# Performance work log

Hardware: AMD Instinct MI355X
Metric: run time of the kernel (lower is better)

The kernel has to match this reference:

```python
import jax, jax.numpy as jnp
import numpy as np

DATA_WIDTH = 416.0
IOU_THRESH = 0.5
TOPK = 1024  # fixed-size candidate set to keep shapes static (replaces dynamic nonzero/filter)


def setup_inputs() -> dict:
    key = jax.random.key(0)
    ks = jax.random.split(key, 6)
    B, C = 32, 255  # 3 anchors * (5 + 80 classes)
    return {
        "out_13": jax.random.normal(ks[0], (B, C, 13, 13), jnp.float32),
        "out_26": jax.random.normal(ks[1], (B, C, 26, 26), jnp.float32),
        "out_52": jax.random.normal(ks[2], (B, C, 52, 52), jnp.float32),
        "thresh_value": jnp.float32(0.0),
        "case": jnp.float32(1.0),
        "anchors_13": jax.random.uniform(ks[3], (3, 2), jnp.float32) * 100.0 + 10.0,
        "anchors_26": jax.random.uniform(ks[4], (3, 2), jnp.float32) * 50.0 + 5.0,
        "anchors_52": jax.random.uniform(ks[5], (3, 2), jnp.float32) * 25.0 + 2.0,
    }


def _decode(out, thresh, anchors, t, case):
    # out: [B, 3*(5+nc), G, G] -> [B, G, G, 3, 5+nc]  (matches permute+reshape in _filter)
    B, ch, G, _ = out.shape
    out = jnp.transpose(out, (0, 2, 3, 1)).reshape(B, G, G, 3, -1)
    conf = jax.nn.sigmoid(out[..., 0])                         # sigmoid(p)
    iy = jnp.arange(G, dtype=out.dtype)[None, :, None, None]   # idxs[:,1]
    ix = jnp.arange(G, dtype=out.dtype)[None, None, :, None]   # idxs[:,2]
    # NOTE: original code uses vecs[:, 2] for BOTH cy and cx (replicated faithfully)
    cy = (iy + out[..., 2]) * t / case
    cx = (ix + out[..., 2]) * t / case
    w = anchors[:, 0] * jnp.exp(out[..., 3]) / case            # broadcast over anchor dim
    h = anchors[:, 1] * jnp.exp(out[..., 4]) / case
    cls_p = jax.nn.softmax(out[..., 5:], axis=-1)
    cls = jnp.argmax(cls_p, axis=-1).astype(out.dtype)
    n = jnp.broadcast_to(jnp.arange(B, dtype=out.dtype)[:, None, None, None], conf.shape)
    boxes = jnp.stack([n, conf, cx, cy, w, h, cls], axis=-1).reshape(-1, 7)
    # threshold filter (mask = sigmoid(p) > thresh), expressed as masked score for static shapes
    score = jnp.where(conf > thresh, conf, -1.0).reshape(-1)
    return boxes, score


def _nms_keep(boxes, score):
    # boxes: [K, 7] rows [n, p, cx, cy, w, h, cls]; greedy NMS, IoU = inter/union ('inter' mode)
    K = boxes.shape[0]
    cx, cy, w, h = boxes[:, 2], boxes[:, 3], boxes[:, 4], boxes[:, 5]
    x1, y1, x2, y2 = cx - w / 2, cy - h / 2, cx + w / 2, cy + h / 2
    area = w * h
    iw = jnp.clip(jnp.minimum(x2[:, None], x2[None, :]) - jnp.maximum(x1[:, None], x1[None, :]), 0.0)
    ih = jnp.clip(jnp.minimum(y2[:, None], y2[None, :]) - jnp.maximum(y1[:, None], y1[None, :]), 0.0)
    inter = iw * ih
    iou = inter / (area[:, None] + area[None, :] - inter + 1e-9)
    idx = jnp.arange(K)
    supp0 = score <= 0.0  # padding / below-threshold entries start suppressed

    def body(i, supp):
        row = (~supp[i]) & (iou[i] > IOU_THRESH) & (idx > i)
        return supp | row

    supp = jax.lax.fori_loop(0, K, body, supp0)
    return ~supp


def reference(out_13, out_26, out_52, thresh_value, case, anchors_13, anchors_26, anchors_52):
    b13, s13 = _decode(out_13, thresh_value, anchors_13, DATA_WIDTH / 13, case)
    b26, s26 = _decode(out_26, thresh_value, anchors_26, DATA_WIDTH / 26, case)
    b52, s52 = _decode(out_52, thresh_value, anchors_52, DATA_WIDTH / 52, case)
    boxes = jnp.concatenate([b13, b26, b52], axis=0)
    score = jnp.concatenate([s13, s26, s52], axis=0)
    topv, topi = jax.lax.top_k(score, TOPK)          # confidence-sorted candidates
    boxes_k = boxes[topi]
    keep = jax.lax.stop_gradient(_nms_keep(boxes_k, topv))
    return boxes_k * keep[:, None].astype(boxes_k.dtype)  # [TOPK, 7], suppressed rows zeroed
```

## Files before the change

kernel.cpp:

```cpp
#include <hip/hip_runtime.h>
#include <math.h>

typedef unsigned int u32;
typedef unsigned long long u64;

#define N_13 16224
#define N_26 64896
#define N_52 259584
#define N_TOT 340704
#define KSEL 1024
#define NBINS 8192
#define NBH 64
#define CAND 2048

#define WS_HIST 0UL
#define WS_STK  32768UL
#define WS_CAND 32784UL
#define WS_GATH 49168UL
#define WS_BOX7 57360UL
#define WS_X1   86032UL
#define WS_Y1   90128UL
#define WS_X2   94224UL
#define WS_Y2   98320UL
#define WS_AR   102416UL
#define WS_SUP  106512UL
#define WS_MASK 110608UL

__device__ __forceinline__ float sigmoid_(float x) {
  return 1.0f / (1.0f + expf(-x));
}

__device__ __forceinline__ u32 fkey_(float f) {
  u32 u = __float_as_uint(f);
  return (u & 0x80000000u) ? ~u : (u | 0x80000000u);
}

__device__ __forceinline__ int binof_(float l0, float score) {
  if (score == -1.0f) return 0;
  int b = (int)floorf((l0 + 8.0f) * 512.0f);
  return b < 0 ? 0 : (b > NBINS-1 ? NBINS-1 : b);
}

__device__ __forceinline__ const float* level_(int t, const float* f13,
                                               const float* f26, const float* f52,
                                               int& G2, int& off, int& tl) {
  if (t < N_13)            { G2 = 169;  off = 0;         tl = t;                return f13; }
  else if (t < N_13+N_26)  { G2 = 676;  off = N_13;      tl = t - N_13;         return f26; }
  else                     { G2 = 2704; off = N_13+N_26; tl = t - (N_13+N_26);  return f52; }
}

__global__ __launch_bounds__(1024) void hist_kernel(const float* __restrict__ f13,
                                                    const float* __restrict__ f26,
                                                    const float* __restrict__ f52,
                                                    const float* __restrict__ thr_p,
                                                    u32* __restrict__ hist) {
  __shared__ u32 lh[NBINS];
  int tid = threadIdx.x;
  for (int i = tid; i < NBINS; i += 1024) lh[i] = 0u;
  __syncthreads();
  float thr = *thr_p;
  for (int t = blockIdx.x * 1024 + tid; t < N_TOT; t += NBH * 1024) {
    int G2, off, tl;
    const float* fp = level_(t, f13, f26, f52, G2, off, tl);
    int p = tl % G2; int c = tl / G2; int a = c % 3; int b = c / 3;
    float l0 = fp[(size_t)(b*255 + a*85) * G2 + p];
    float conf = sigmoid_(l0);
    float score = (conf > thr) ? conf : -1.0f;
    atomicAdd(&lh[binof_(l0, score)], 1u);
  }
  __syncthreads();
  for (int i = tid; i < NBINS; i += 1024) {
    u32 v = lh[i];
    if (v) atomicAdd(&hist[i], v);
  }
}

__global__ __launch_bounds__(1024) void pick_kernel(const u32* __restrict__ hist,
                                                    u32* __restrict__ stk,
                                                    u64* __restrict__ cand) {
  __shared__ u32 lh[NBINS];
  __shared__ u32 suf[1024];
  int t = threadIdx.x;
  u32 s = 0;
  #pragma unroll 8
  for (int d = 0; d < 8; ++d) { u32 v = hist[t*8 + d]; lh[t*8 + d] = v; s += v; }
  suf[t] = s;
  __syncthreads();
  for (int off = 1; off < 1024; off <<= 1) {
    u32 v = (t + off < 1024) ? suf[t + off] : 0u;
    __syncthreads();
    suf[t] += v;
    __syncthreads();
  }
  if (suf[t] >= (u32)KSEL && (t == 1023 || suf[t+1] < (u32)KSEL)) {
    u32 cum = (t < 1023) ? suf[t+1] : 0u;
    int bsel = t*8;
    for (int d = 7; d >= 0; --d) {
      cum += lh[t*8 + d];
      if (cum >= (u32)KSEL) { bsel = t*8 + d; break; }
    }
    stk[1] = (u32)bsel;
  }
  cand[t] = 0ull; cand[t + 1024] = 0ull;
}

__global__ void gather_kernel(const float* __restrict__ f13,
                              const float* __restrict__ f26,
                              const float* __restrict__ f52,
                              const float* __restrict__ thr_p,
                              u32* __restrict__ stk, u64* __restrict__ cand) {
  int t = blockIdx.x * blockDim.x + threadIdx.x;
  if (t >= N_TOT) return;
  float thr = *thr_p;
  int G2, off, tl;
  const float* fp = level_(t, f13, f26, f52, G2, off, tl);
  int p = tl % G2; int c = tl / G2; int a = c % 3; int b = c / 3;
  float l0 = fp[(size_t)(b*255 + a*85) * G2 + p];
  float conf = sigmoid_(l0);
  float score = (conf > thr) ? conf : -1.0f;
  int bin = binof_(l0, score);
  if ((u32)bin >= stk[1]) {
    u32 iref = (u32)(off + (b*G2 + p)*3 + a);
    u64 key = ((u64)fkey_(score) << 19) | (u64)(524287u - iref);
    u32 pos = atomicAdd(&stk[0], 1u);
    if (pos < (u32)CAND) cand[pos] = key;
  }
}

__global__ __launch_bounds__(1024) void sort_kernel(const u64* __restrict__ cand,
                                                    u64* __restrict__ gath) {
  __shared__ u64 sk[CAND];
  int t = threadIdx.x;
  sk[t] = cand[t]; sk[t + 1024] = cand[t + 1024];
  __syncthreads();
  for (int kk = 2; kk <= CAND; kk <<= 1) {
    for (int j = kk >> 1; j > 0; j >>= 1) {
      #pragma unroll
      for (int h = 0; h < 2; ++h) {
        int e = t + h*1024;
        int ixj = e ^ j;
        if (ixj > e) {
          u64 x0 = sk[e], x1 = sk[ixj];
          bool descRegion = (e & kk) == 0;
          bool sw = descRegion ? (x0 < x1) : (x0 > x1);
          if (sw) { sk[e] = x1; sk[ixj] = x0; }
        }
      }
      __syncthreads();
    }
  }
  gath[t] = sk[t];
}

__global__ void decode_kernel(const float* __restrict__ f13,
                              const float* __restrict__ f26,
                              const float* __restrict__ f52,
                              const float* __restrict__ a13,
                              const float* __restrict__ a26,
                              const float* __restrict__ a52,
                              const float* __restrict__ case_p,
                              const u64* __restrict__ gath,
                              float* __restrict__ box7,
                              float* __restrict__ bx1, float* __restrict__ by1,
                              float* __restrict__ bx2, float* __restrict__ by2,
                              float* __restrict__ bar, u32* __restrict__ bsup) {
  int gt = blockIdx.x * blockDim.x + threadIdx.x;
  int r = gt >> 6;
  int lane = gt & 63;
  if (r >= KSEL) return;
  u64 key = gath[r];
  u32 idx = 524287u - ((u32)key & 0x7FFFFu);
  u32 sb = (u32)(key >> 19);
  sb = (sb & 0x80000000u) ? (sb & 0x7FFFFFFFu) : ~sb;
  float score = __uint_as_float(sb);
  float case_v = *case_p;

  const float* fp; const float* ap; u32 G, G2, off; float tt;
  if (idx < N_13)            { fp=f13; ap=a13; G=13; G2=169;  off=0;          tt=32.0f; }
  else if (idx < N_13+N_26)  { fp=f26; ap=a26; G=26; G2=676;  off=N_13;       tt=16.0f; }
  else                       { fp=f52; ap=a52; G=52; G2=2704; off=N_13+N_26;  tt=8.0f;  }
  u32 L = idx - off;
  u32 a = L % 3u; u32 q = L / 3u;
  u32 x = q % G; u32 rq = q / G; u32 y = rq % G; u32 b = rq / G;

  const float* base = fp + (size_t)(b*255u + a*85u) * G2 + y*G + x;
  float l0 = base[0];
  float conf = sigmoid_(l0);
  float l2 = base[(size_t)2*G2];
  float l3 = base[(size_t)3*G2];
  float l4 = base[(size_t)4*G2];
  float cy = ((float)y + l2) * tt / case_v;
  float cx = ((float)x + l2) * tt / case_v;
  float w = ap[2*a]     * expf(l3) / case_v;
  float h = ap[2*a + 1] * expf(l4) / case_v;

  bool v2ok = (lane < 16);
  float x1 = base[(size_t)(5 + lane) * G2];
  float x2 = v2ok ? base[(size_t)(5 + 64 + lane) * G2] : -INFINITY;
  float mx = fmaxf(x1, x2);
  #pragma unroll
  for (int o = 32; o > 0; o >>= 1) mx = fmaxf(mx, __shfl_xor(mx, o));
  float e1 = expf(x1 - mx);
  float e2 = v2ok ? expf(x2 - mx) : 0.0f;
  float ssum = e1 + e2;
  #pragma unroll
  for (int o = 32; o > 0; o >>= 1) ssum += __shfl_xor(ssum, o);
  float p1 = e1 / ssum;
  float p2 = v2ok ? (e2 / ssum) : -1.0f;
  float pm = p1; int ci = lane;
  if (p2 > pm) { pm = p2; ci = lane + 64; }
  #pragma unroll
  for (int o = 32; o > 0; o >>= 1) {
    float om = __shfl_xor(pm, o);
    int   oc = __shfl_xor(ci, o);
    if (om > pm || (om == pm && oc < ci)) { pm = om; ci = oc; }
  }

  if (lane == 0) {
    box7[r*7 + 0] = (float)b;
    box7[r*7 + 1] = conf;
    box7[r*7 + 2] = cx;
    box7[r*7 + 3] = cy;
    box7[r*7 + 4] = w;
    box7[r*7 + 5] = h;
    box7[r*7 + 6] = (float)ci;
    float hw = __fmul_rn(w, 0.5f);
    float hh = __fmul_rn(h, 0.5f);
    bx1[r] = __fsub_rn(cx, hw);
    bx2[r] = __fadd_rn(cx, hw);
    by1[r] = __fsub_rn(cy, hh);
    by2[r] = __fadd_rn(cy, hh);
    bar[r] = __fmul_rn(w, h);
    bsup[r] = (score <= 0.0f) ? 1u : 0u;
  }
}

__global__ __launch_bounds__(256) void mask_kernel(const float* __restrict__ bx1,
                                                   const float* __restrict__ by1,
                                                   const float* __restrict__ bx2,
                                                   const float* __restrict__ by2,
                                                   const float* __restrict__ bar,
                                                   u64* __restrict__ mask) {
  __shared__ float sx1[1024], sy1[1024], sx2[1024], sy2[1024], sar[1024];
  int t = threadIdx.x;
  for (int k = t; k < 1024; k += 256) {
    sx1[k] = bx1[k]; sy1[k] = by1[k];
    sx2[k] = bx2[k]; sy2[k] = by2[k]; sar[k] = bar[k];
  }
  __syncthreads();
  int T = blockIdx.x * 256 + t;
  int i = T >> 4, w = T & 15;
  float x1 = sx1[i], y1 = sy1[i], x2 = sx2[i], y2 = sy2[i], ar = sar[i];
  u64 m = 0;
  int j0 = w << 6;
  for (int b = 0; b < 64; ++b) {
    int j = j0 + b;
    float iw = fmaxf(__fsub_rn(fminf(sx2[j], x2), fmaxf(sx1[j], x1)), 0.0f);
    float ih = fmaxf(__fsub_rn(fminf(sy2[j], y2), fmaxf(sy1[j], y1)), 0.0f);
    float inter = __fmul_rn(iw, ih);
    float den = __fadd_rn(__fsub_rn(__fadd_rn(ar, sar[j]), inter), 1e-9f);
    float iou = inter / den;
    if (iou > 0.5f && j > i) m |= (1ull << b);
  }
  mask[i*16 + w] = m;
}

__global__ __launch_bounds__(1024) void resolve_kernel(const u64* __restrict__ mask,
                                                       const u32* __restrict__ bsup,
                                                       const float* __restrict__ box7,
                                                       float* __restrict__ out) {
  __shared__ u64 sm[16384];
  __shared__ u64 ssupw[16];
  int t = threadIdx.x;
  for (int k = t; k < 16384; k += 1024) sm[k] = mask[k];
  __syncthreads();
  if (t < 64) {
    int lane = t;
    u64 supp = 0;
    for (int w = 0; w < 16; ++w) {
      u64 bal = __ballot(bsup[w*64 + lane] != 0u);
      if (w == lane) supp = bal;
    }
    u64 c0, c1, c2, c3, n0, n1, n2, n3;
    c0 = (lane < 16) ? sm[0*16 + lane] : 0ull;
    c1 = (lane < 16) ? sm[1*16 + lane] : 0ull;
    c2 = (lane < 16) ? sm[2*16 + lane] : 0ull;
    c3 = (lane < 16) ? sm[3*16 + lane] : 0ull;
    for (int i = 0; i < 1024; i += 4) {
      if (i + 4 < 1024) {
        n0 = (lane < 16) ? sm[(i+4)*16 + lane] : 0ull;
        n1 = (lane < 16) ? sm[(i+5)*16 + lane] : 0ull;
        n2 = (lane < 16) ? sm[(i+6)*16 + lane] : 0ull;
        n3 = (lane < 16) ? sm[(i+7)*16 + lane] : 0ull;
      } else { n0 = n1 = n2 = n3 = 0ull; }
      u64 sw;
      sw = __shfl(supp, (i  ) >> 6); if (!((sw >> ((i  ) & 63)) & 1ull)) supp |= c0;
      sw = __shfl(supp, (i+1) >> 6); if (!((sw >> ((i+1) & 63)) & 1ull)) supp |= c1;
      sw = __shfl(supp, (i+2) >> 6); if (!((sw >> ((i+2) & 63)) & 1ull)) supp |= c2;
      sw = __shfl(supp, (i+3) >> 6); if (!((sw >> ((i+3) & 63)) & 1ull)) supp |= c3;
      c0 = n0; c1 = n1; c2 = n2; c3 = n3;
    }
    if (lane < 16) ssupw[lane] = supp;
  }
  __syncthreads();
  u32 keep = !((ssupw[t >> 6] >> (t & 63)) & 1ull);
  #pragma unroll
  for (int c = 0; c < 7; ++c) {
    float v = box7[t*7 + c];
    out[t*7 + c] = keep ? v : 0.0f;
  }
}

extern "C" void kernel_launch(void* const* d_in, const int* in_sizes, int n_in,
                              void* d_out, int out_size, void* d_ws, size_t ws_size,
                              hipStream_t stream) {
  const float* f13 = (const float*)d_in[0];
  const float* f26 = (const float*)d_in[1];
  const float* f52 = (const float*)d_in[2];
  const float* thr = (const float*)d_in[3];
  const float* cas = (const float*)d_in[4];
  const float* a13 = (const float*)d_in[5];
  const float* a26 = (const float*)d_in[6];
  const float* a52 = (const float*)d_in[7];
  float* out = (float*)d_out;
  char* ws = (char*)d_ws;

  u32* hist = (u32*)(ws + WS_HIST);
  u32* stk  = (u32*)(ws + WS_STK);
  u64* cand = (u64*)(ws + WS_CAND);
  u64* gath = (u64*)(ws + WS_GATH);
  float* box7 = (float*)(ws + WS_BOX7);
  float* bx1 = (float*)(ws + WS_X1);
  float* by1 = (float*)(ws + WS_Y1);
  float* bx2 = (float*)(ws + WS_X2);
  float* by2 = (float*)(ws + WS_Y2);
  float* bar = (float*)(ws + WS_AR);
  u32* bsup = (u32*)(ws + WS_SUP);
  u64* mask = (u64*)(ws + WS_MASK);

  const int nb = (N_TOT + 255) / 256;

  hipMemsetAsync(ws + WS_HIST, 0, 32768 + 16, stream);
  hist_kernel<<<NBH, 1024, 0, stream>>>(f13, f26, f52, thr, hist);
  pick_kernel<<<1, 1024, 0, stream>>>(hist, stk, cand);
  gather_kernel<<<nb, 256, 0, stream>>>(f13, f26, f52, thr, stk, cand);
  sort_kernel<<<1, 1024, 0, stream>>>(cand, gath);
  decode_kernel<<<256, 256, 0, stream>>>(f13, f26, f52, a13, a26, a52, cas, gath,
                                         box7, bx1, by1, bx2, by2, bar, bsup);
  mask_kernel<<<64, 256, 0, stream>>>(bx1, by1, bx2, by2, bar, mask);
  resolve_kernel<<<1, 1024, 0, stream>>>(mask, bsup, box7, out);
}
```

Measured before the change: 281.4 us.

## Fuse NMS pipeline into single cooperative kernel with grid syncs

Replaces seven kernel launches and a memset with one cooperative kernel of 64 blocks that separates the stages with grid.sync. The bitonic sort becomes a parallel rank-by-count sort spread across blocks. The resolve step now works on 32-bit words using readlane, and the histogram loops are specialised per level through templates. The aim is to remove launch and inter-kernel gaps; the cost is grid-wide barriers and having the whole pipeline use only 64 blocks.

```diff
diff --git a/kernel.cpp b/kernel.cpp
--- a/kernel.cpp
+++ b/kernel.cpp
@@ -1,5 +1,8 @@
 #include <hip/hip_runtime.h>
+#include <hip/hip_cooperative_groups.h>
 #include <math.h>
+
+namespace cg = cooperative_groups;
 
 typedef unsigned int u32;
 typedef unsigned long long u64;
@@ -10,8 +13,10 @@
 #define N_TOT 340704
 #define KSEL 1024
 #define NBINS 8192
-#define NBH 64
 #define CAND 2048
+#define NBLK 64
+#define NTHR 1024
+#define GSTRIDE (NBLK * NTHR)
 
 #define WS_HIST 0UL
 #define WS_STK  32768UL
@@ -41,273 +46,271 @@
   return b < 0 ? 0 : (b > NBINS-1 ? NBINS-1 : b);
 }
 
-__device__ __forceinline__ const float* level_(int t, const float* f13,
-                                               const float* f26, const float* f52,
-                                               int& G2, int& off, int& tl) {
-  if (t < N_13)            { G2 = 169;  off = 0;         tl = t;                return f13; }
-  else if (t < N_13+N_26)  { G2 = 676;  off = N_13;      tl = t - N_13;         return f26; }
-  else                     { G2 = 2704; off = N_13+N_26; tl = t - (N_13+N_26);  return f52; }
-}
-
-__global__ __launch_bounds__(1024) void hist_kernel(const float* __restrict__ f13,
-                                                    const float* __restrict__ f26,
-                                                    const float* __restrict__ f52,
-                                                    const float* __restrict__ thr_p,
-                                                    u32* __restrict__ hist) {
-  __shared__ u32 lh[NBINS];
-  int tid = threadIdx.x;
-  for (int i = tid; i < NBINS; i += 1024) lh[i] = 0u;
-  __syncthreads();
-  float thr = *thr_p;
-  for (int t = blockIdx.x * 1024 + tid; t < N_TOT; t += NBH * 1024) {
-    int G2, off, tl;
-    const float* fp = level_(t, f13, f26, f52, G2, off, tl);
-    int p = tl % G2; int c = tl / G2; int a = c % 3; int b = c / 3;
-    float l0 = fp[(size_t)(b*255 + a*85) * G2 + p];
-    float conf = sigmoid_(l0);
-    float score = (conf > thr) ? conf : -1.0f;
-    atomicAdd(&lh[binof_(l0, score)], 1u);
-  }
-  __syncthreads();
-  for (int i = tid; i < NBINS; i += 1024) {
-    u32 v = lh[i];
-    if (v) atomicAdd(&hist[i], v);
-  }
-}
-
-__global__ __launch_bounds__(1024) void pick_kernel(const u32* __restrict__ hist,
-                                                    u32* __restrict__ stk,
-                                                    u64* __restrict__ cand) {
-  __shared__ u32 lh[NBINS];
-  __shared__ u32 suf[1024];
-  int t = threadIdx.x;
-  u32 s = 0;
-  #pragma unroll 8
-  for (int d = 0; d < 8; ++d) { u32 v = hist[t*8 + d]; lh[t*8 + d] = v; s += v; }
-  suf[t] = s;
-  __syncthreads();
-  for (int off = 1; off < 1024; off <<= 1) {
-    u32 v = (t + off < 1024) ? suf[t + off] : 0u;
-    __syncthreads();
-    suf[t] += v;
-    __syncthreads();
-  }
-  if (suf[t] >= (u32)KSEL && (t == 1023 || suf[t+1] < (u32)KSEL)) {
-    u32 cum = (t < 1023) ? suf[t+1] : 0u;
-    int bsel = t*8;
-    for (int d = 7; d >= 0; --d) {
-      cum += lh[t*8 + d];
-      if (cum >= (u32)KSEL) { bsel = t*8 + d; break; }
-    }
-    stk[1] = (u32)bsel;
-  }
-  cand[t] = 0ull; cand[t + 1024] = 0ull;
-}
-
-__global__ void gather_kernel(const float* __restrict__ f13,
-                              const float* __restrict__ f26,
-                              const float* __restrict__ f52,
-                              const float* __restrict__ thr_p,
-                              u32* __restrict__ stk, u64* __restrict__ cand) {
-  int t = blockIdx.x * blockDim.x + threadIdx.x;
-  if (t >= N_TOT) return;
-  float thr = *thr_p;
-  int G2, off, tl;
-  const float* fp = level_(t, f13, f26, f52, G2, off, tl);
-  int p = tl % G2; int c = tl / G2; int a = c % 3; int b = c / 3;
+template<int G2>
+__device__ __forceinline__ void hist_item(const float* __restrict__ fp, int u,
+                                          float thr, u32* lh) {
+  int p = u % G2; int c = u / G2; int a = c % 3; int b = c / 3;
+  float l0 = fp[(size_t)(b*255 + a*85) * G2 + p];
+  float conf = sigmoid_(l0);
+  float score = (conf > thr) ? conf : -1.0f;
+  atomicAdd(&lh[binof_(l0, score)], 1u);
+}
+
+template<int G2, int OFF>
+__device__ __forceinline__ void gather_item(const float* __restrict__ fp, int u,
+                                            float thr, u32 bsel,
+                                            u32* stk, u64* cand) {
+  int p = u % G2; int c = u / G2; int a = c % 3; int b = c / 3;
   float l0 = fp[(size_t)(b*255 + a*85) * G2 + p];
   float conf = sigmoid_(l0);
   float score = (conf > thr) ? conf : -1.0f;
   int bin = binof_(l0, score);
-  if ((u32)bin >= stk[1]) {
-    u32 iref = (u32)(off + (b*G2 + p)*3 + a);
+  if ((u32)bin >= bsel) {
+    u32 iref = (u32)(OFF + (b*G2 + p)*3 + a);
     u64 key = ((u64)fkey_(score) << 19) | (u64)(524287u - iref);
     u32 pos = atomicAdd(&stk[0], 1u);
     if (pos < (u32)CAND) cand[pos] = key;
   }
 }
 
-__global__ __launch_bounds__(1024) void sort_kernel(const u64* __restrict__ cand,
-                                                    u64* __restrict__ gath) {
-  __shared__ u64 sk[CAND];
-  int t = threadIdx.x;
-  sk[t] = cand[t]; sk[t + 1024] = cand[t + 1024];
+union SmemT {
+  u32 lh[NBINS];
+  u32 wsum[16];
+  u64 sk[CAND];
+  struct { float x1[1024], y1[1024], x2[1024], y2[1024], ar[1024]; } mk;
+  struct { u32 sm32[33280]; u32 sw[32]; } rs;
+};
+
+__global__ __launch_bounds__(NTHR) void fused_kernel(
+    const float* __restrict__ f13, const float* __restrict__ f26,
+    const float* __restrict__ f52, const float* __restrict__ thr_p,
+    const float* __restrict__ case_p, const float* __restrict__ a13,
+    const float* __restrict__ a26, const float* __restrict__ a52,
+    float* __restrict__ out, char* __restrict__ ws) {
+  __shared__ SmemT sm;
+  cg::grid_group grid = cg::this_grid();
+
+  u32* hist = (u32*)(ws + WS_HIST);
+  u32* stk  = (u32*)(ws + WS_STK);
+  u64* cand = (u64*)(ws + WS_CAND);
+  u64* gath = (u64*)(ws + WS_GATH);
+  float* box7 = (float*)(ws + WS_BOX7);
+  float* bx1 = (float*)(ws + WS_X1);
+  float* by1 = (float*)(ws + WS_Y1);
+  float* bx2 = (float*)(ws + WS_X2);
+  float* by2 = (float*)(ws + WS_Y2);
+  float* bar = (float*)(ws + WS_AR);
+  u32* bsup = (u32*)(ws + WS_SUP);
+  u64* mask = (u64*)(ws + WS_MASK);
+
+  const int tid = threadIdx.x;
+  const int gtid = blockIdx.x * NTHR + tid;
+
+  for (int i = tid; i < NBINS; i += NTHR) sm.lh[i] = 0u;
   __syncthreads();
-  for (int kk = 2; kk <= CAND; kk <<= 1) {
-    for (int j = kk >> 1; j > 0; j >>= 1) {
+  if (gtid < NBINS) hist[gtid] = 0u;
+  if (gtid < 4) stk[gtid] = 0u;
+  if (gtid < CAND) cand[gtid] = 0ull;
+  {
+    float thr = *thr_p;
+    for (int u = gtid; u < N_13; u += GSTRIDE) hist_item<169 >(f13, u, thr, sm.lh);
+    for (int u = gtid; u < N_26; u += GSTRIDE) hist_item<676 >(f26, u, thr, sm.lh);
+    for (int u = gtid; u < N_52; u += GSTRIDE) hist_item<2704>(f52, u, thr, sm.lh);
+  }
+  __syncthreads();
+  grid.sync();
+
+  for (int i = tid; i < NBINS; i += NTHR) {
+    u32 v = sm.lh[i];
+    if (v) atomicAdd(&hist[i], v);
+  }
+  grid.sync();
+
+  if (blockIdx.x == 0) {
+    u32 h[8]; u32 s = 0;
+    #pragma unroll
+    for (int d = 0; d < 8; ++d) { h[d] = hist[tid*8 + d]; s += h[d]; }
+    u32 r = s;
+    #pragma unroll
+    for (int off = 1; off < 64; off <<= 1) {
+      u32 v = __shfl_down(r, off);
+      if ((tid & 63) + off < 64) r += v;
+    }
+    if ((tid & 63) == 0) sm.wsum[tid >> 6] = r;
+    __syncthreads();
+    u32 add = 0;
+    for (int w2 = (tid >> 6) + 1; w2 < 16; ++w2) add += sm.wsum[w2];
+    u32 suf = r + add;
+    if (suf >= (u32)KSEL && (suf - s) < (u32)KSEL) {
+      u32 cum = suf - s;
+      int bsel = tid*8;
+      for (int d = 7; d >= 0; --d) {
+        cum += h[d];
+        if (cum >= (u32)KSEL) { bsel = tid*8 + d; break; }
+      }
+      stk[1] = (u32)bsel;
+    }
+  }
+  grid.sync();
+
+  {
+    float thr = *thr_p;
+    u32 bsel = stk[1];
+    for (int u = gtid; u < N_13; u += GSTRIDE) gather_item<169 , 0          >(f13, u, thr, bsel, stk, cand);
+    for (int u = gtid; u < N_26; u += GSTRIDE) gather_item<676 , N_13      >(f26, u, thr, bsel, stk, cand);
+    for (int u = gtid; u < N_52; u += GSTRIDE) gather_item<2704, N_13+N_26 >(f52, u, thr, bsel, stk, cand);
+  }
+  grid.sync();
+
+  {
+    for (int k = tid; k < CAND; k += NTHR) sm.sk[k] = cand[k];
+    __syncthreads();
+    int e = blockIdx.x * 32 + (tid >> 5);
+    int sub = tid & 31;
+    u64 mykey = sm.sk[e];
+    u32 cnt = 0;
+    for (int s = 0; s < 64; ++s) {
+      int j = sub*64 + ((s + sub) & 63);
+      cnt += (sm.sk[j] > mykey) ? 1u : 0u;
+    }
+    #pragma unroll
+    for (int off = 1; off < 32; off <<= 1) cnt += __shfl_xor(cnt, off);
+    if (sub == 0 && cnt < (u32)KSEL) gath[cnt] = mykey;
+  }
+  grid.sync();
+
+  {
+    int r = blockIdx.x * 16 + (tid >> 6);
+    int lane = tid & 63;
+    u64 key = gath[r];
+    u32 idx = 524287u - ((u32)key & 0x7FFFFu);
+    u32 sb = (u32)(key >> 19);
+    sb = (sb & 0x80000000u) ? (sb & 0x7FFFFFFFu) : ~sb;
+    float score = __uint_as_float(sb);
+    float case_v = *case_p;
+
+    const float* fp; const float* ap; u32 G, G2, off; float tt;
+    if (idx < N_13)            { fp=f13; ap=a13; G=13; G2=169;  off=0;          tt=32.0f; }
+    else if (idx < N_13+N_26)  { fp=f26; ap=a26; G=26; G2=676;  off=N_13;       tt=16.0f; }
+    else                       { fp=f52; ap=a52; G=52; G2=2704; off=N_13+N_26;  tt=8.0f;  }
+    u32 L = idx - off;
+    u32 a = L % 3u; u32 q = L / 3u;
+    u32 x = q % G; u32 rq = q / G; u32 y = rq % G; u32 b = rq / G;
+
+    const float* base = fp + (size_t)(b*255u + a*85u) * G2 + y*G + x;
+    float l0 = base[0];
+    float conf = sigmoid_(l0);
+    float l2 = base[(size_t)2*G2];
+    float l3 = base[(size_t)3*G2];
+    float l4 = base[(size_t)4*G2];
+    float cy = ((float)y + l2) * tt / case_v;
+    float cx = ((float)x + l2) * tt / case_v;
+    float w = ap[2*a]     * expf(l3) / case_v;
+    float h = ap[2*a + 1] * expf(l4) / case_v;
+
+    bool v2ok = (lane < 16);
+    float x1v = base[(size_t)(5 + lane) * G2];
+    float x2v = v2ok ? base[(size_t)(5 + 64 + lane) * G2] : -INFINITY;
+    float mx = fmaxf(x1v, x2v);
+    #pragma unroll
+    for (int o = 32; o > 0; o >>= 1) mx = fmaxf(mx, __shfl_xor(mx, o));
+    float e1 = expf(x1v - mx);
+    float e2 = v2ok ? expf(x2v - mx) : 0.0f;
+    float ssum = e1 + e2;
+    #pragma unroll
+    for (int o = 32; o > 0; o >>= 1) ssum += __shfl_xor(ssum, o);
+    float p1 = e1 / ssum;
+    float p2 = v2ok ? (e2 / ssum) : -1.0f;
+    float pm = p1; int ci = lane;
+    if (p2 > pm) { pm = p2; ci = lane + 64; }
+    #pragma unroll
+    for (int o = 32; o > 0; o >>= 1) {
+      float om = __shfl_xor(pm, o);
+      int   oc = __shfl_xor(ci, o);
+      if (om > pm || (om == pm && oc < ci)) { pm = om; ci = oc; }
+    }
+
+    if (lane == 0) {
+      box7[r*7 + 0] = (float)b;
+      box7[r*7 + 1] = conf;
+      box7[r*7 + 2] = cx;
+      box7[r*7 + 3] = cy;
+      box7[r*7 + 4] = w;
+      box7[r*7 + 5] = h;
+      box7[r*7 + 6] = (float)ci;
+      float hw = __fmul_rn(w, 0.5f);
+      float hh = __fmul_rn(h, 0.5f);
+      bx1[r] = __fsub_rn(cx, hw);
+      bx2[r] = __fadd_rn(cx, hw);
+      by1[r] = __fsub_rn(cy, hh);
+      by2[r] = __fadd_rn(cy, hh);
+      bar[r] = __fmul_rn(w, h);
+      bsup[r] = (score <= 0.0f) ? 1u : 0u;
+    }
+  }
+  grid.sync();
+
+  if (blockIdx.x < 16) {
+    sm.mk.x1[tid] = bx1[tid]; sm.mk.y1[tid] = by1[tid];
+    sm.mk.x2[tid] = bx2[tid]; sm.mk.y2[tid] = by2[tid];
+    sm.mk.ar[tid] = bar[tid];
+    __syncthreads();
+    int P = blockIdx.x * NTHR + tid;
+    int i = P >> 4, w = P & 15;
+    float x1 = sm.mk.x1[i], y1 = sm.mk.y1[i];
+    float x2 = sm.mk.x2[i], y2 = sm.mk.y2[i], ar = sm.mk.ar[i];
+    u64 m = 0;
+    int j0 = w << 6;
+    for (int b = 0; b < 64; ++b) {
+      int j = j0 + b;
+      float iw = fmaxf(__fsub_rn(fminf(sm.mk.x2[j], x2), fmaxf(sm.mk.x1[j], x1)), 0.0f);
+      float ih = fmaxf(__fsub_rn(fminf(sm.mk.y2[j], y2), fmaxf(sm.mk.y1[j], y1)), 0.0f);
+      float inter = __fmul_rn(iw, ih);
+      float den = __fadd_rn(__fsub_rn(__fadd_rn(ar, sm.mk.ar[j]), inter), 1e-9f);
+      float iou = inter / den;
+      if (iou > 0.5f && j > i) m |= (1ull << b);
+    }
+    mask[i*16 + w] = m;
+  }
+  grid.sync();
+
+  if (blockIdx.x == 0) {
+    u64* smask = (u64*)sm.rs.sm32;
+    for (int k = tid; k < 16384; k += NTHR) smask[k] = mask[k];
+    if (tid < 256) smask[16384 + tid] = 0ull;
+    if (tid < 32) sm.rs.sw[tid] = 0u;
+    __syncthreads();
+    if (bsup[tid]) atomicOr(&sm.rs.sw[tid >> 5], 1u << (tid & 31));
+    __syncthreads();
+    if (tid < 64) {
+      int lane = tid;
+      bool act = lane < 32;
+      u32 supp = act ? sm.rs.sw[lane] : 0u;
+      u32 cur[8], nxt[8];
       #pragma unroll
-      for (int h = 0; h < 2; ++h) {
-        int e = t + h*1024;
-        int ixj = e ^ j;
-        if (ixj > e) {
-          u64 x0 = sk[e], x1 = sk[ixj];
-          bool descRegion = (e & kk) == 0;
-          bool sw = descRegion ? (x0 < x1) : (x0 > x1);
-          if (sw) { sk[e] = x1; sk[ixj] = x0; }
+      for (int k = 0; k < 8; ++k) cur[k] = act ? sm.rs.sm32[k*32 + lane] : 0u;
+      for (int blk = 0; blk < 128; ++blk) {
+        #pragma unroll
+        for (int k = 0; k < 8; ++k)
+          nxt[k] = act ? sm.rs.sm32[(blk*8 + 8 + k)*32 + lane] : 0u;
+        #pragma unroll
+        for (int k = 0; k < 8; ++k) {
+          int i = blk*8 + k;
+          u32 swd = (u32)__builtin_amdgcn_readlane((int)supp, i >> 5);
+          if (!((swd >> (i & 31)) & 1u)) supp |= cur[k];
         }
+        #pragma unroll
+        for (int k = 0; k < 8; ++k) cur[k] = nxt[k];
       }
-      __syncthreads();
-    }
-  }
-  gath[t] = sk[t];
-}
-
-__global__ void decode_kernel(const float* __restrict__ f13,
-                              const float* __restrict__ f26,
-                              const float* __restrict__ f52,
-                              const float* __restrict__ a13,
-                              const float* __restrict__ a26,
-                              const float* __restrict__ a52,
-                              const float* __restrict__ case_p,
-                              const u64* __restrict__ gath,
-                              float* __restrict__ box7,
-                              float* __restrict__ bx1, float* __restrict__ by1,
-                              float* __restrict__ bx2, float* __restrict__ by2,
-                              float* __restrict__ bar, u32* __restrict__ bsup) {
-  int gt = blockIdx.x * blockDim.x + threadIdx.x;
-  int r = gt >> 6;
-  int lane = gt & 63;
-  if (r >= KSEL) return;
-  u64 key = gath[r];
-  u32 idx = 524287u - ((u32)key & 0x7FFFFu);
-  u32 sb = (u32)(key >> 19);
-  sb = (sb & 0x80000000u) ? (sb & 0x7FFFFFFFu) : ~sb;
-  float score = __uint_as_float(sb);
-  float case_v = *case_p;
-
-  const float* fp; const float* ap; u32 G, G2, off; float tt;
-  if (idx < N_13)            { fp=f13; ap=a13; G=13; G2=169;  off=0;          tt=32.0f; }
-  else if (idx < N_13+N_26)  { fp=f26; ap=a26; G=26; G2=676;  off=N_13;       tt=16.0f; }
-  else                       { fp=f52; ap=a52; G=52; G2=2704; off=N_13+N_26;  tt=8.0f;  }
-  u32 L = idx - off;
-  u32 a = L % 3u; u32 q = L / 3u;
-  u32 x = q % G; u32 rq = q / G; u32 y = rq % G; u32 b = rq / G;
-
-  const float* base = fp + (size_t)(b*255u + a*85u) * G2 + y*G + x;
-  float l0 = base[0];
-  float conf = sigmoid_(l0);
-  float l2 = base[(size_t)2*G2];
-  float l3 = base[(size_t)3*G2];
-  float l4 = base[(size_t)4*G2];
-  float cy = ((float)y + l2) * tt / case_v;
-  float cx = ((float)x + l2) * tt / case_v;
-  float w = ap[2*a]     * expf(l3) / case_v;
-  float h = ap[2*a + 1] * expf(l4) / case_v;
-
-  bool v2ok = (lane < 16);
-  float x1 = base[(size_t)(5 + lane) * G2];
-  float x2 = v2ok ? base[(size_t)(5 + 64 + lane) * G2] : -INFINITY;
-  float mx = fmaxf(x1, x2);
-  #pragma unroll
-  for (int o = 32; o > 0; o >>= 1) mx = fmaxf(mx, __shfl_xor(mx, o));
-  float e1 = expf(x1 - mx);
-  float e2 = v2ok ? expf(x2 - mx) : 0.0f;
-  float ssum = e1 + e2;
-  #pragma unroll
-  for (int o = 32; o > 0; o >>= 1) ssum += __shfl_xor(ssum, o);
-  float p1 = e1 / ssum;
-  float p2 = v2ok ? (e2 / ssum) : -1.0f;
-  float pm = p1; int ci = lane;
-  if (p2 > pm) { pm = p2; ci = lane + 64; }
-  #pragma unroll
-  for (int o = 32; o > 0; o >>= 1) {
-    float om = __shfl_xor(pm, o);
-    int   oc = __shfl_xor(ci, o);
-    if (om > pm || (om == pm && oc < ci)) { pm = om; ci = oc; }
-  }
-
-  if (lane == 0) {
-    box7[r*7 + 0] = (float)b;
-    box7[r*7 + 1] = conf;
-    box7[r*7 + 2] = cx;
-    box7[r*7 + 3] = cy;
-    box7[r*7 + 4] = w;
-    box7[r*7 + 5] = h;
-    box7[r*7 + 6] = (float)ci;
-    float hw = __fmul_rn(w, 0.5f);
-    float hh = __fmul_rn(h, 0.5f);
-    bx1[r] = __fsub_rn(cx, hw);
-    bx2[r] = __fadd_rn(cx, hw);
-    by1[r] = __fsub_rn(cy, hh);
-    by2[r] = __fadd_rn(cy, hh);
-    bar[r] = __fmul_rn(w, h);
-    bsup[r] = (score <= 0.0f) ? 1u : 0u;
-  }
-}
-
-__global__ __launch_bounds__(256) void mask_kernel(const float* __restrict__ bx1,
-                                                   const float* __restrict__ by1,
-                                                   const float* __restrict__ bx2,
-                                                   const float* __restrict__ by2,
-                                                   const float* __restrict__ bar,
-                                                   u64* __restrict__ mask) {
-  __shared__ float sx1[1024], sy1[1024], sx2[1024], sy2[1024], sar[1024];
-  int t = threadIdx.x;
-  for (int k = t; k < 1024; k += 256) {
-    sx1[k] = bx1[k]; sy1[k] = by1[k];
-    sx2[k] = bx2[k]; sy2[k] = by2[k]; sar[k] = bar[k];
-  }
-  __syncthreads();
-  int T = blockIdx.x * 256 + t;
-  int i = T >> 4, w = T & 15;
-  float x1 = sx1[i], y1 = sy1[i], x2 = sx2[i], y2 = sy2[i], ar = sar[i];
-  u64 m = 0;
-  int j0 = w << 6;
-  for (int b = 0; b < 64; ++b) {
-    int j = j0 + b;
-    float iw = fmaxf(__fsub_rn(fminf(sx2[j], x2), fmaxf(sx1[j], x1)), 0.0f);
-    float ih = fmaxf(__fsub_rn(fminf(sy2[j], y2), fmaxf(sy1[j], y1)), 0.0f);
-    float inter = __fmul_rn(iw, ih);
-    float den = __fadd_rn(__fsub_rn(__fadd_rn(ar, sar[j]), inter), 1e-9f);
-    float iou = inter / den;
-    if (iou > 0.5f && j > i) m |= (1ull << b);
-  }
-  mask[i*16 + w] = m;
-}
-
-__global__ __launch_bounds__(1024) void resolve_kernel(const u64* __restrict__ mask,
-                                                       const u32* __restrict__ bsup,
-                                                       const float* __restrict__ box7,
-                                                       float* __restrict__ out) {
-  __shared__ u64 sm[16384];
-  __shared__ u64 ssupw[16];
-  int t = threadIdx.x;
-  for (int k = t; k < 16384; k += 1024) sm[k] = mask[k];
-  __syncthreads();
-  if (t < 64) {
-    int lane = t;
-    u64 supp = 0;
-    for (int w = 0; w < 16; ++w) {
-      u64 bal = __ballot(bsup[w*64 + lane] != 0u);
-      if (w == lane) supp = bal;
-    }
-    u64 c0, c1, c2, c3, n0, n1, n2, n3;
-    c0 = (lane < 16) ? sm[0*16 + lane] : 0ull;
-    c1 = (lane < 16) ? sm[1*16 + lane] : 0ull;
-    c2 = (lane < 16) ? sm[2*16 + lane] : 0ull;
-    c3 = (lane < 16) ? sm[3*16 + lane] : 0ull;
-    for (int i = 0; i < 1024; i += 4) {
-      if (i + 4 < 1024) {
-        n0 = (lane < 16) ? sm[(i+4)*16 + lane] : 0ull;
-        n1 = (lane < 16) ? sm[(i+5)*16 + lane] : 0ull;
-        n2 = (lane < 16) ? sm[(i+6)*16 + lane] : 0ull;
-        n3 = (lane < 16) ? sm[(i+7)*16 + lane] : 0ull;
-      } else { n0 = n1 = n2 = n3 = 0ull; }
-      u64 sw;
-      sw = __shfl(supp, (i  ) >> 6); if (!((sw >> ((i  ) & 63)) & 1ull)) supp |= c0;
-      sw = __shfl(supp, (i+1) >> 6); if (!((sw >> ((i+1) & 63)) & 1ull)) supp |= c1;
-      sw = __shfl(supp, (i+2) >> 6); if (!((sw >> ((i+2) & 63)) & 1ull)) supp |= c2;
-      sw = __shfl(supp, (i+3) >> 6); if (!((sw >> ((i+3) & 63)) & 1ull)) supp |= c3;
-      c0 = n0; c1 = n1; c2 = n2; c3 = n3;
-    }
-    if (lane < 16) ssupw[lane] = supp;
-  }
-  __syncthreads();
-  u32 keep = !((ssupw[t >> 6] >> (t & 63)) & 1ull);
-  #pragma unroll
-  for (int c = 0; c < 7; ++c) {
-    float v = box7[t*7 + c];
-    out[t*7 + c] = keep ? v : 0.0f;
+      if (act) sm.rs.sw[lane] = supp;
+    }
+    __syncthreads();
+    u32 keep = !((sm.rs.sw[tid >> 5] >> (tid & 31)) & 1u);
+    #pragma unroll
+    for (int c = 0; c < 7; ++c) {
+      float v = box7[tid*7 + c];
+      out[tid*7 + c] = keep ? v : 0.0f;
+    }
   }
 }
 
@@ -325,28 +328,9 @@
   float* out = (float*)d_out;
   char* ws = (char*)d_ws;
 
-  u32* hist = (u32*)(ws + WS_HIST);
-  u32* stk  = (u32*)(ws + WS_STK);
-  u64* cand = (u64*)(ws + WS_CAND);
-  u64* gath = (u64*)(ws + WS_GATH);
-  float* box7 = (float*)(ws + WS_BOX7);
-  float* bx1 = (float*)(ws + WS_X1);
-  float* by1 = (float*)(ws + WS_Y1);
-  float* bx2 = (float*)(ws + WS_X2);
-  float* by2 = (float*)(ws + WS_Y2);
-  float* bar = (float*)(ws + WS_AR);
-  u32* bsup = (u32*)(ws + WS_SUP);
-  u64* mask = (u64*)(ws + WS_MASK);
-
-  const int nb = (N_TOT + 255) / 256;
-
-  hipMemsetAsync(ws + WS_HIST, 0, 32768 + 16, stream);
-  hist_kernel<<<NBH, 1024, 0, stream>>>(f13, f26, f52, thr, hist);
-  pick_kernel<<<1, 1024, 0, stream>>>(hist, stk, cand);
-  gather_kernel<<<nb, 256, 0, stream>>>(f13, f26, f52, thr, stk, cand);
-  sort_kernel<<<1, 1024, 0, stream>>>(cand, gath);
-  decode_kernel<<<256, 256, 0, stream>>>(f13, f26, f52, a13, a26, a52, cas, gath,
-                                         box7, bx1, by1, bx2, by2, bar, bsup);
-  mask_kernel<<<64, 256, 0, stream>>>(bx1, by1, bx2, by2, bar, mask);
-  resolve_kernel<<<1, 1024, 0, stream>>>(mask, bsup, box7, out);
-}
+  void* args[] = { (void*)&f13, (void*)&f26, (void*)&f52, (void*)&thr,
+                   (void*)&cas, (void*)&a13, (void*)&a26, (void*)&a52,
+                   (void*)&out, (void*)&ws };
+  hipLaunchCooperativeKernel((void*)fused_kernel, dim3(NBLK), dim3(NTHR),
+                             args, 0, stream);
+}
```

New measurement: 338.2 us. 1.2x slower.
